# Optimization experiments

Hardware: AMD Instinct MI355X
Metric: run time of the kernel (lower is better)

Reference implementation:

```python
import jax, jax.numpy as jnp
import numpy as np

SHOT, WAY, DIM, Q, R = 5, 32, 640, 4096, 10
TEMP, L, DIV = 16.0, 2.0, 10.0
EPS = 1e-5


def _expmap0(x, c):
    # x: (..., d); c: broadcastable to (..., 1). Exponential map at origin + ball projection.
    sc = jnp.sqrt(c)
    n = jnp.maximum(jnp.linalg.norm(x, axis=-1, keepdims=True), EPS)
    y = jnp.tanh(sc * n) * x / (sc * n)
    ny = jnp.maximum(jnp.linalg.norm(y, axis=-1, keepdims=True), EPS)
    maxn = (1.0 - 1e-3) / sc
    return jnp.where(ny > maxn, y * (maxn / ny), y)


def _dist(x, y, c):
    # Poincare distance: 2/sqrt(c) * artanh(sqrt(c) * ||mobius_add(-x, y)||)
    u = -x
    uy = jnp.sum(u * y, -1, keepdims=True)
    u2 = jnp.sum(u * u, -1, keepdims=True)
    y2 = jnp.sum(y * y, -1, keepdims=True)
    num = (1.0 + 2.0 * c * uy + c * y2) * u + (1.0 - c * u2) * y
    den = jnp.maximum(1.0 + 2.0 * c * uy + c * c * u2 * y2, EPS)
    n = jnp.linalg.norm(num / den, axis=-1, keepdims=True)
    sc = jnp.sqrt(c)
    arg = jnp.clip(sc * n, 0.0, 1.0 - EPS)
    return ((2.0 / sc) * jnp.arctanh(arg))[..., 0]


def setup_inputs() -> dict:
    key = jax.random.key(0)
    ks = jax.random.split(key, 8)
    f = lambda k, s: jax.random.normal(k, s, dtype=jnp.float32)
    z = lambda s: jnp.zeros(s, jnp.float32)
    return {
        "data_shot": f(ks[0], (SHOT * WAY, DIM)),
        "data_query": f(ks[1], (Q, DIM)),
        "W1": f(ks[2], (2 * DIM, 128)) * 0.05, "b1": z((128,)),
        "W2": f(ks[3], (128, 64)) * 0.05, "b2": z((64,)),
        "W3": f(ks[4], (64, 5)) * 0.05, "b3": z((5,)),
        "Wr1": f(ks[5], (2 * R + 2, R)) * 0.05, "br1": z((R,)),
        "Wr2": f(ks[6], (R, R + 1)) * 0.05, "br2": z((R + 1,)),
    }


def reference(data_shot, data_query, W1, b1, W2, b2, W3, b3, Wr1, br1, Wr2, br2):
    # --- episode stats + per-class curvature controller ---
    all_data = jnp.concatenate([data_shot, data_query], 0).mean(0)      # (dim,)
    protos = data_shot.reshape(SHOT, WAY, DIM).mean(0)                  # (way, dim)
    ctrl_in = jnp.concatenate([protos, jnp.broadcast_to(all_data, (WAY, DIM))], 1)
    h = jax.nn.relu(ctrl_in @ W1 + b1)
    h = jax.nn.relu(h @ W2 + b2)
    cand = jnp.arange(1, 6, dtype=jnp.float32) * (L / DIV)              # 5 curvature candidates
    c = jax.nn.softmax(h @ W3 + b3, axis=-1) @ cand                     # (way,) positive curvature

    # --- hyperbolic projection + per-class proto-query distances (vectorized over classes) ---
    proto_p = _expmap0(protos, c[:, None])                              # (way, dim)
    query_p = _expmap0(data_query[None], c[:, None, None])              # (way, Q, dim)
    dis_mat = _dist(proto_p[:, None, :], query_p, c[:, None, None])     # (way, Q)

    # --- sort + gather-based rerank features ---
    idx = jnp.argsort(dis_mat, axis=1)
    idx_near, idx_far = idx[:, :R], idx[:, R:]
    n_i_d = jnp.take_along_axis(dis_mat, idx_near, 1)                   # (way, R)
    o_i_d = jnp.take_along_axis(dis_mat, idx_far, 1).mean(1)            # (way,)
    dT = dis_mat.T                                                      # (Q, way)
    Gnear = dT[idx_near]                                                # (way, R, way): [i,k,j] = dis_mat[j, idx_near[i,k]]
    n_o_d = (Gnear.sum(-1) - n_i_d) / (WAY - 1)                         # (way, R)
    Gfar = dT[idx_far]                                                  # (way, Q-R, way)
    ii = jnp.arange(WAY)
    mlt = (ii[None, :] < ii[:, None]).astype(dis_mat.dtype)             # j < i
    mgt = (ii[None, :] > ii[:, None]).astype(dis_mat.dtype)             # j > i
    sumA = jnp.einsum('ikj,ij->i', Gfar, mlt)                           # gathered cols (rows before i)
    sumB = mgt @ dis_mat[:, R:].sum(1)                                  # raw cols R: (rows after i, as in source)
    o_o_d = (sumA + sumB) / ((WAY - 1) * (Q - R))

    # --- rerank controller MLP ---
    rr_in = jnp.concatenate([n_i_d, n_o_d, o_i_d[:, None], o_o_d[:, None]], 1)  # (way, 2R+2)
    hr = jax.nn.relu(rr_in @ Wr1 + br1)
    orr = hr @ Wr2 + br2                                                # (way, R+1)
    i_w = jax.nn.softmax(orr[:, :R], axis=-1)                           # (way, R)
    onw = jax.nn.sigmoid(orr[:, R])                                     # (way,)

    # --- proto update + final distances ---
    near_q = data_query[idx_near]                                       # (way, R, dim)
    wdq = (near_q * i_w[:, :, None]).sum(1)                             # (way, dim)
    tmp = protos * onw[:, None] + wdq * (1.0 - onw[:, None])
    test_proto = _expmap0(tmp, c[:, None])
    new_dis = _dist(test_proto[:, None, :], query_p, c[:, None, None])  # (way, Q)
    return -new_dis.T / TEMP                                            # (Q, way)
```

## Files before the change

kernel.cpp:

```cpp
#include <hip/hip_runtime.h>
#include <math.h>

#define NSHOT 5
#define WAY 32
#define DIM 640
#define NQ 4096
#define RNEAR 10

constexpr int OFF_PROTOS = 0;
constexpr int OFF_QPART  = 20480;
constexpr int OFF_C      = 102400;
constexpr int OFF_BETA   = 102432;
constexpr int OFF_S      = 102464;
constexpr int OFF_U      = 102496;
constexpr int OFF_NID    = 102528;
constexpr int OFF_RR     = 102848;
constexpr int OFF_SPC    = 103552;
constexpr int OFF_H1P    = 103584;
constexpr int OFF_TP     = 107680;
constexpr int OFF_G      = 128160;
constexpr int OFF_NIDX   = 259232;
constexpr int OFF_Q2D    = 259556;
constexpr int OFF_X2D    = 267748;
constexpr int OFF_X2D2   = 267812;
constexpr int OFF_P2RAW  = 267876;
constexpr int OFF_H1PART = 268000;

__device__ __forceinline__ double wave_sum_d(double v) {
#pragma unroll
  for (int o = 32; o > 0; o >>= 1) v += __shfl_down(v, o, 64);
  return v;
}

__device__ __forceinline__ double dist_hyp(double c, double xdotq, double u2, double q2) {
  const double EPSd = 1e-5;
  double sc = sqrt(c);
  double nq = sqrt(q2);
  double nf = fmax(nq, EPSd);
  double th = tanh(sc * nf);
  double al = th / (sc * nf);
  double ny = fmax(al * nq, EPSd);
  double mx = 0.999 / sc;
  if (ny > mx) al *= mx / ny;
  double y2 = al * al * q2;
  double uy = -al * xdotq;
  double A = 1.0 + 2.0 * c * uy + c * y2;
  double B = 1.0 - c * u2;
  double den = fmax(1.0 + 2.0 * c * uy + c * c * u2 * y2, EPSd);
  double num2 = fmax(A * A * u2 + 2.0 * A * B * uy + B * B * y2, 0.0);
  double n = sqrt(num2) / den;
  double arg = sc * n;
  const double CLIP = (double)(1.0f - 1e-5f);
  arg = fmin(fmax(arg, 0.0), CLIP);
  return (1.0 / sc) * log((1.0 + arg) / (1.0 - arg));
}

__device__ __forceinline__ float dist_f32(float c, float xdotq, float u2, float q2) {
  const float EPSf = 1e-5f;
  float sc = sqrtf(c);
  float nq = sqrtf(q2);
  float nf = fmaxf(nq, EPSf);
  float th = tanhf(sc * nf);
  float al = th / (sc * nf);
  float ny = fmaxf(al * nq, EPSf);
  float mx = 0.999f / sc;
  if (ny > mx) al *= mx / ny;
  float y2 = al * al * q2;
  float uy = -al * xdotq;
  float A = 1.f + 2.f * c * uy + c * y2;
  float B = 1.f - c * u2;
  float den = fmaxf(1.f + 2.f * c * uy + c * c * u2 * y2, EPSf);
  float num2 = fmaxf(A * A * u2 + 2.f * A * B * uy + B * B * y2, 0.f);
  float n = sqrtf(num2) / den;
  float arg = sc * n;
  arg = fminf(fmaxf(arg, 0.f), 1.f - 1e-5f);
  return (1.f / sc) * logf((1.f + arg) / (1.f - arg));
}

__device__ __forceinline__ double expmap_scale(double c, double p2, double* u2out) {
  double sc = sqrt(c);
  double ntrue = sqrt(p2);
  double nf = fmax(ntrue, 1e-5);
  double th = tanh(sc * nf);
  double s0 = th / (sc * nf);
  double ny = fmax(s0 * ntrue, 1e-5);
  double mx = 0.999 / sc;
  if (ny > mx) s0 *= mx / ny;
  *u2out = s0 * s0 * p2;
  return s0;
}

__global__ __launch_bounds__(640) void k_fuse1(const float* __restrict__ Qm,
                                               const float* __restrict__ shot,
                                               const float* __restrict__ W1, float* ws) {
  __shared__ double q2w[32][10];
  __shared__ double psred[10];
  __shared__ float pr[DIM];
  __shared__ float h1pp[5][128];
  int b = blockIdx.x, t = threadIdx.x;
  int lane = t & 63, wid = t >> 6;
  float protoval = 0.f;
  if (b < WAY) {
    float s = 0.f;
#pragma unroll
    for (int s5 = 0; s5 < NSHOT; ++s5) s += shot[(size_t)(s5 * WAY + b) * DIM + t];
    protoval = s * 0.2f;
    pr[t] = protoval;
    ws[OFF_PROTOS + b * DIM + t] = protoval;
    double pv2 = (double)protoval * protoval;
    pv2 = wave_sum_d(pv2);
    if (lane == 0) psred[wid] = pv2;
  }
  int r0 = b * 32;
  float colacc = 0.f;
  for (int r = 0; r < 32; ++r) {
    float v = Qm[(size_t)(r0 + r) * DIM + t];
    colacc += v;
    double sq = (double)v * v;
    sq = wave_sum_d(sq);
    if (lane == 0) q2w[r][wid] = sq;
  }
  ws[OFF_QPART + b * DIM + t] = colacc + 5.f * protoval;
  __syncthreads();
  if (t < 32) {
    double s = 0.0;
#pragma unroll
    for (int k = 0; k < 10; ++k) s += q2w[t][k];
    ((double*)(ws + OFF_Q2D))[r0 + t] = s;
  }
  if (b < WAY) {
    int n = t & 127, s = t >> 7;
    int k0 = s * 128;
    float acc = 0.f;
#pragma unroll 8
    for (int k = k0; k < k0 + 128; ++k) acc = fmaf(pr[k], W1[(size_t)k * 128 + n], acc);
    h1pp[s][n] = acc;
    __syncthreads();
    if (t < 128)
      ws[OFF_H1P + b * 128 + t] = h1pp[0][t] + h1pp[1][t] + h1pp[2][t] + h1pp[3][t] + h1pp[4][t];
    if (t == 0) {
      double p2 = 0.0;
#pragma unroll
      for (int k = 0; k < 10; ++k) p2 += psred[k];
      ((double*)(ws + OFF_P2RAW))[b] = p2;
    }
  }
}

__global__ __launch_bounds__(320) void k_amw1(const float* __restrict__ W1, float* ws) {
  __shared__ float part_am[4][80];
  __shared__ float am_s[80];
  __shared__ float h1part[2][128];
  int j = blockIdx.x, t = threadIdx.x;
  {
    int c = t % 80, pg = t / 80;
    const float* base = ws + OFF_QPART + j * 80 + c;
    int p0 = pg * 32;
    float a0 = 0.f, a1 = 0.f, a2 = 0.f, a3 = 0.f;
#pragma unroll 8
    for (int p = 0; p < 32; p += 4) {
      a0 += base[(size_t)(p0 + p + 0) * DIM];
      a1 += base[(size_t)(p0 + p + 1) * DIM];
      a2 += base[(size_t)(p0 + p + 2) * DIM];
      a3 += base[(size_t)(p0 + p + 3) * DIM];
    }
    part_am[pg][c] = (a0 + a1) + (a2 + a3);
  }
  __syncthreads();
  if (t < 80)
    am_s[t] = (part_am[0][t] + part_am[1][t] + part_am[2][t] + part_am[3][t]) * (1.f / 4256.f);
  __syncthreads();
  if (t < 256) {
    int n = t & 127, kh = t >> 7;
    int kbase = j * 80 + kh * 40;
    float acc = 0.f;
#pragma unroll 8
    for (int k = 0; k < 40; ++k)
      acc = fmaf(am_s[kh * 40 + k], W1[(size_t)(DIM + kbase + k) * 128 + n], acc);
    h1part[kh][n] = acc;
  }
  __syncthreads();
  if (t < 128) ws[OFF_H1PART + j * 128 + t] = h1part[0][t] + h1part[1][t];
}

__global__ __launch_bounds__(128) void k_ctrl2(const float* __restrict__ b1,
                                               const float* __restrict__ W2, const float* __restrict__ b2,
                                               const float* __restrict__ W3, const float* __restrict__ b3,
                                               float* ws) {
  __shared__ float h1s[128];
  __shared__ float h2p[2][64];
  __shared__ float h2s[64], lg[5];
  int w = blockIdx.x, t = threadIdx.x;
  {
    float a = ws[OFF_H1P + w * 128 + t] + b1[t];
#pragma unroll
    for (int j = 0; j < 8; ++j) a += ws[OFF_H1PART + j * 128 + t];
    h1s[t] = fmaxf(a, 0.f);
  }
  __syncthreads();
  {
    int n = t & 63, kh = t >> 6;
    int k0 = kh * 64;
    float acc = 0.f;
#pragma unroll 8
    for (int k = 0; k < 64; ++k)
      acc = fmaf(h1s[k0 + k], W2[(size_t)(k0 + k) * 64 + n], acc);
    h2p[kh][n] = acc;
  }
  __syncthreads();
  if (t < 64) h2s[t] = fmaxf(h2p[0][t] + h2p[1][t] + b2[t], 0.f);
  __syncthreads();
  if (t < 5) {
    float acc = b3[t];
    for (int k = 0; k < 64; ++k) acc = fmaf(h2s[k], W3[k * 5 + t], acc);
    lg[t] = acc;
  }
  __syncthreads();
  if (t == 0) {
    double m = lg[0];
    for (int i = 1; i < 5; ++i) m = fmax(m, (double)lg[i]);
    double se = 0.0, cv = 0.0;
    for (int i = 0; i < 5; ++i) { double e = exp((double)lg[i] - m); se += e; cv += e * 0.2 * (double)(i + 1); }
    double c = cv / se;
    ws[OFF_C + w] = (float)c;
    double p2 = ((const double*)(ws + OFF_P2RAW))[w];
    double u2;
    double beta = expmap_scale(c, p2, &u2);
    ws[OFF_BETA + w] = (float)beta;
    ((double*)(ws + OFF_X2D))[w] = u2;
  }
}

#define GEMM_COMPUTE2(BUF)                                            \
  {                                                                   \
    const float* qr = &S[BUF][q][0];                                  \
    const float* x0r = &S[BUF][16 + w0][0];                           \
    const float* x1r = &S[BUF][16 + w1][0];                           \
    _Pragma("unroll")                                                 \
    for (int kk = 0; kk < 64; kk += 4) {                              \
      float4 qv = *(const float4*)(qr + kk);                          \
      float4 x0v = *(const float4*)(x0r + kk);                        \
      float4 x1v = *(const float4*)(x1r + kk);                       \
      c0x = fmaf(qv.x, x0v.x, c0x); c0y = fmaf(qv.y, x0v.y, c0y);     \
      c0z = fmaf(qv.z, x0v.z, c0z); c0w = fmaf(qv.w, x0v.w, c0w);     \
      c1x = fmaf(qv.x, x1v.x, c1x); c1y = fmaf(qv.y, x1v.y, c1y);     \
      c1z = fmaf(qv.z, x1v.z, c1z); c1w = fmaf(qv.w, x1v.w, c1w);     \
    }                                                                 \
  }

__global__ __launch_bounds__(256) void k_gemm(const float* __restrict__ X, const float* __restrict__ Qm,
                                              float* __restrict__ ws, int mode, float* __restrict__ out) {
  __shared__ float S[2][48][68];
  int t = threadIdx.x;
  int q0 = blockIdx.x * 16;
  int rr = t >> 4, qd = t & 15;
  const float* srcA = Qm + (size_t)(q0 + rr) * DIM + qd * 4;
  const float* srcB = X + (size_t)rr * DIM + qd * 4;
  const float* srcC = X + (size_t)(rr + 16) * DIM + qd * 4;
  float4 a0 = *(const float4*)srcA;
  float4 a1 = *(const float4*)srcB;
  float4 a2 = *(const float4*)srcC;
  *(float4*)&S[0][rr][qd * 4] = a0;
  *(float4*)&S[0][16 + rr][qd * 4] = a1;
  *(float4*)&S[0][32 + rr][qd * 4] = a2;
  __syncthreads();
  a0 = *(const float4*)(srcA + 64);
  a1 = *(const float4*)(srcB + 64);
  a2 = *(const float4*)(srcC + 64);
  float4 b0 = {0.f,0.f,0.f,0.f}, b1 = b0, b2 = b0;
  int q = t & 15, wp = t >> 4;
  int w0 = wp * 2, w1 = wp * 2 + 1;
  float c0x = 0.f, c0y = 0.f, c0z = 0.f, c0w = 0.f;
  float c1x = 0.f, c1y = 0.f, c1z = 0.f, c1w = 0.f;
#pragma unroll
  for (int c = 0; c < 10; c += 2) {
    GEMM_COMPUTE2(0)
    if (c + 2 < 10) {
      size_t kc = (size_t)(c + 2) * 64;
      b0 = *(const float4*)(srcA + kc);
      b1 = *(const float4*)(srcB + kc);
      b2 = *(const float4*)(srcC + kc);
    }
    if (c + 1 < 10) {
      *(float4*)&S[1][rr][qd * 4] = a0;
      *(float4*)&S[1][16 + rr][qd * 4] = a1;
      *(float4*)&S[1][32 + rr][qd * 4] = a2;
      __syncthreads();
      GEMM_COMPUTE2(1)
      if (c + 3 < 10) {
        size_t kc = (size_t)(c + 3) * 64;
        a0 = *(const float4*)(srcA + kc);
        a1 = *(const float4*)(srcB + kc);
        a2 = *(const float4*)(srcC + kc);
      }
      if (c + 2 < 10) {
        *(float4*)&S[0][rr][qd * 4] = b0;
        *(float4*)&S[0][16 + rr][qd * 4] = b1;
        *(float4*)&S[0][32 + rr][qd * 4] = b2;
        __syncthreads();
      }
    }
  }
  float acc0 = (c0x + c0y) + (c0z + c0w);
  float acc1 = (c1x + c1y) + (c1z + c1w);
  int qq = q0 + q;
  const double* q2d = (const double*)(ws + OFF_Q2D);
  if (mode == 0) {
    const double* x2d = (const double*)(ws + OFF_X2D);
    float q2f = (float)q2d[qq];
    float d0 = dist_f32(ws[OFF_C + w0], ws[OFF_BETA + w0] * acc0, (float)x2d[w0], q2f);
    float d1 = dist_f32(ws[OFF_C + w1], ws[OFF_BETA + w1] * acc1, (float)x2d[w1], q2f);
    ws[OFF_G + (size_t)w0 * NQ + qq] = d0;
    ws[OFF_G + (size_t)w1 * NQ + qq] = d1;
  } else {
    const double* u2arr = (const double*)(ws + OFF_X2D2);
    double q2 = q2d[qq];
    double d0 = dist_hyp((double)ws[OFF_C + w0], (double)acc0, u2arr[w0], q2);
    double d1 = dist_hyp((double)ws[OFF_C + w1], (double)acc1, u2arr[w1], q2);
    out[(size_t)qq * WAY + w0] = (float)(-d0 / 16.0);
    out[(size_t)qq * WAY + w1] = (float)(-d1 / 16.0);
  }
}

__global__ __launch_bounds__(1024) void k_topkA(float* __restrict__ ws) {
  __shared__ double sredS[16], sredU[16];
  __shared__ float cval[160];
  __shared__ int cidx[160];
  __shared__ float qvsh[RNEAR];
  __shared__ int qjsh[RNEAR];
  __shared__ float colsh[RNEAR][33];
  __shared__ float pcpart[RNEAR];
  int w = blockIdx.x, t = threadIdx.x;
  int lane = t & 63, wid = t >> 6;
  int* nidx = (int*)(ws + OFF_NIDX);
  const float* gb = ws + OFF_G + (size_t)w * NQ;
  float v0 = gb[t], v1 = gb[1024 + t], v2 = gb[2048 + t], v3 = gb[3072 + t];
  unsigned tk = 0;
  double s = (double)v0 + (double)v1 + (double)v2 + (double)v3;
  double u = (t < RNEAR) ? (double)v0 : 0.0;
  s = wave_sum_d(s);
  u = wave_sum_d(u);
  if (lane == 0) { sredS[wid] = s; sredU[wid] = u; }
  for (int r = 0; r < RNEAR; ++r) {
    float lv = INFINITY; int li = 0x7fffffff;
    if (!(tk & 1u) && (v0 < lv || (v0 == lv && t < li)))        { lv = v0; li = t; }
    if (!(tk & 2u) && (v1 < lv || (v1 == lv && 1024 + t < li))) { lv = v1; li = 1024 + t; }
    if (!(tk & 4u) && (v2 < lv || (v2 == lv && 2048 + t < li))) { lv = v2; li = 2048 + t; }
    if (!(tk & 8u) && (v3 < lv || (v3 == lv && 3072 + t < li))) { lv = v3; li = 3072 + t; }
#pragma unroll
    for (int o = 32; o > 0; o >>= 1) {
      float ov = __shfl_xor(lv, o, 64);
      int oi = __shfl_xor(li, o, 64);
      if (ov < lv || (ov == lv && oi < li)) { lv = ov; li = oi; }
    }
    if (lane == 0) { cval[wid * RNEAR + r] = lv; cidx[wid * RNEAR + r] = li; }
    if ((li & 1023) == t) tk |= 1u << (li >> 10);
  }
  __syncthreads();
  if (t == 0) {
    double S = 0.0, U = 0.0;
    for (int k = 0; k < 16; ++k) { S += sredS[k]; U += sredU[k]; }
    ws[OFF_S + w] = (float)S;
    ws[OFF_U + w] = (float)U;
  }
  if (t < 64) {
    float c0 = cval[t], c1 = cval[t + 64];
    int i0 = cidx[t], i1 = cidx[t + 64];
    float c2 = (t < 32) ? cval[t + 128] : INFINITY;
    int i2 = (t < 32) ? cidx[t + 128] : 0x7fffffff;
    unsigned m = 0;
    for (int r = 0; r < RNEAR; ++r) {
      float lv = INFINITY; int li = 0x7fffffff;
      if (!(m & 1u) && (c0 < lv || (c0 == lv && i0 < li))) { lv = c0; li = i0; }
      if (!(m & 2u) && (c1 < lv || (c1 == lv && i1 < li))) { lv = c1; li = i1; }
      if (!(m & 4u) && (c2 < lv || (c2 == lv && i2 < li))) { lv = c2; li = i2; }
#pragma unroll
      for (int o = 32; o > 0; o >>= 1) {
        float ov = __shfl_xor(lv, o, 64);
        int oi = __shfl_xor(li, o, 64);
        if (ov < lv || (ov == lv && oi < li)) { lv = ov; li = oi; }
      }
      if (lane == 0) { qvsh[r] = lv; qjsh[r] = li; }
      if (i0 == li) m |= 1u;
      if (i1 == li) m |= 2u;
      if (i2 == li) m |= 4u;
    }
  }
  __syncthreads();
  if (t < WAY * RNEAR) {
    int j = t >> 5, w2 = t & 31;
    colsh[j][w2] = ws[OFF_G + (size_t)w2 * NQ + qjsh[j]];
  }
  __syncthreads();
  if (t < RNEAR) {
    double cs = 0.0, pc = 0.0;
    for (int w2 = 0; w2 < WAY; ++w2) {
      float dv = colsh[t][w2];
      cs += dv;
      if (w2 < w) pc += dv;
    }
    ws[OFF_RR + w * 22 + t] = qvsh[t];
    ws[OFF_RR + w * 22 + RNEAR + t] = (float)((cs - qvsh[t]) / (double)(WAY - 1));
    ws[OFF_NID + w * RNEAR + t] = qvsh[t];
    nidx[w * RNEAR + t] = qjsh[t];
    pcpart[t] = (float)pc;
  }
  __syncthreads();
  if (t == 0) {
    double spc = 0.0, sn = 0.0;
    for (int j = 0; j < RNEAR; ++j) { spc += pcpart[j]; sn += qvsh[j]; }
    double S = (double)ws[OFF_S + w];
    ws[OFF_RR + w * 22 + 20] = (float)((S - sn) / (double)(NQ - RNEAR));
    ws[OFF_SPC + w] = (float)spc;
  }
}

__global__ __launch_bounds__(640) void k_refB(const float* __restrict__ Qm,
                                              const float* __restrict__ Wr1, const float* __restrict__ br1,
                                              const float* __restrict__ Wr2, const float* __restrict__ br2,
                                              float* __restrict__ ws) {
  __shared__ float Ssh[WAY], Ush[WAY];
  __shared__ float rrl[22];
  __shared__ int qj[RNEAR];
  __shared__ float hr[RNEAR], orsh[11], iw[RNEAR];
  __shared__ float onw_sh;
  __shared__ double p2red[10];
  __shared__ double gshd;
  int w = blockIdx.x, t = threadIdx.x;
  int lane = t & 63, wid = t >> 6;
  const int* nidx = (const int*)(ws + OFF_NIDX);
  if (t < WAY) { Ssh[t] = ws[OFF_S + t]; Ush[t] = ws[OFF_U + t]; }
  if (t >= 64 && t < 64 + 22) rrl[t - 64] = ws[OFF_RR + w * 22 + (t - 64)];
  if (t >= 96 && t < 96 + RNEAR) qj[t - 96] = nidx[w * RNEAR + (t - 96)];
  __syncthreads();
  if (t == 0) {
    double pref = 0.0, suf = 0.0;
    for (int j = 0; j < w; ++j) pref += (double)Ssh[j];
    for (int j = w + 1; j < WAY; ++j) suf += (double)Ssh[j] - (double)Ush[j];
    double spc = (double)ws[OFF_SPC + w];
    rrl[21] = (float)((pref - spc + suf) / ((double)(WAY - 1) * (double)(NQ - RNEAR)));
  }
  __syncthreads();
  if (t < RNEAR) {
    float a = br1[t];
    for (int k = 0; k < 22; ++k) a = fmaf(rrl[k], Wr1[k * RNEAR + t], a);
    hr[t] = fmaxf(a, 0.f);
  }
  __syncthreads();
  if (t < 11) {
    float a = br2[t];
    for (int k = 0; k < RNEAR; ++k) a = fmaf(hr[k], Wr2[k * 11 + t], a);
    orsh[t] = a;
  }
  __syncthreads();
  if (t == 0) {
    double m = orsh[0];
    for (int i = 1; i < RNEAR; ++i) m = fmax(m, (double)orsh[i]);
    double se = 0.0; double e[RNEAR];
    for (int i = 0; i < RNEAR; ++i) { e[i] = exp((double)orsh[i] - m); se += e[i]; }
    for (int i = 0; i < RNEAR; ++i) iw[i] = (float)(e[i] / se);
    onw_sh = (float)(1.0 / (1.0 + exp(-(double)orsh[10])));
  }
  __syncthreads();
  float onwv = onw_sh;
  float wd = 0.f;
#pragma unroll
  for (int j = 0; j < RNEAR; ++j)
    wd = fmaf(Qm[(size_t)qj[j] * DIM + t], iw[j], wd);
  float a0 = ws[OFF_PROTOS + w * DIM + t] * onwv + wd * (1.f - onwv);
  double ls = (double)a0 * a0;
  ls = wave_sum_d(ls);
  if (lane == 0) p2red[wid] = ls;
  __syncthreads();
  if (t == 0) {
    double p2 = 0.0;
#pragma unroll
    for (int k = 0; k < 10; ++k) p2 += p2red[k];
    double u22;
    gshd = expmap_scale((double)ws[OFF_C + w], p2, &u22);
    ((double*)(ws + OFF_X2D2))[w] = u22;
  }
  __syncthreads();
  ws[OFF_TP + w * DIM + t] = (float)gshd * a0;
}

extern "C" void kernel_launch(void* const* d_in, const int* in_sizes, int n_in,
                              void* d_out, int out_size, void* d_ws, size_t ws_size,
                              hipStream_t stream) {
  (void)in_sizes; (void)n_in; (void)out_size; (void)ws_size;
  const float* shot = (const float*)d_in[0];
  const float* qry  = (const float*)d_in[1];
  const float* W1   = (const float*)d_in[2];
  const float* b1   = (const float*)d_in[3];
  const float* W2   = (const float*)d_in[4];
  const float* b2   = (const float*)d_in[5];
  const float* W3   = (const float*)d_in[6];
  const float* b3   = (const float*)d_in[7];
  const float* Wr1  = (const float*)d_in[8];
  const float* br1  = (const float*)d_in[9];
  const float* Wr2  = (const float*)d_in[10];
  const float* br2  = (const float*)d_in[11];
  float* ws = (float*)d_ws;
  float* out = (float*)d_out;

  hipLaunchKernelGGL(k_fuse1, dim3(128), dim3(640), 0, stream, qry, shot, W1, ws);
  hipLaunchKernelGGL(k_amw1,  dim3(8), dim3(320), 0, stream, W1, ws);
  hipLaunchKernelGGL(k_ctrl2, dim3(32), dim3(128), 0, stream, b1, W2, b2, W3, b3, ws);
  hipLaunchKernelGGL(k_gemm,  dim3(256), dim3(256), 0, stream, ws + OFF_PROTOS, qry, ws, 0, out);
  hipLaunchKernelGGL(k_topkA, dim3(32), dim3(1024), 0, stream, ws);
  hipLaunchKernelGGL(k_refB,  dim3(32), dim3(640), 0, stream, qry, Wr1, br1, Wr2, br2, ws);
  hipLaunchKernelGGL(k_gemm,  dim3(256), dim3(256), 0, stream, ws + OFF_TP, qry, ws, 1, out);
}
```

Before: 80.92 us.

## Fuse controller MLP into last-arriving k_amw1 block; use fp32 final distance

Merges the k_ctrl2 kernel into k_amw1 through an atomic arrival counter. The last of the 8 blocks does the layer-2/3 MLP and softmax curvature for all 32 classes, which removes one kernel launch. The final-distance path in the second gemm switches from double-precision dist_hyp to the fp32 dist_f32, cutting costly fp64 transcendentals. The trade-offs are serial tail work in a single block and possible precision loss in the output distances.

```diff
diff --git a/kernel.cpp b/kernel.cpp
--- a/kernel.cpp
+++ b/kernel.cpp
@@ -25,6 +25,7 @@
 constexpr int OFF_X2D2   = 267812;
 constexpr int OFF_P2RAW  = 267876;
 constexpr int OFF_H1PART = 268000;
+constexpr int OFF_CNT    = 269024;
 
 __device__ __forceinline__ double wave_sum_d(double v) {
 #pragma unroll
@@ -32,27 +33,11 @@
   return v;
 }
 
-__device__ __forceinline__ double dist_hyp(double c, double xdotq, double u2, double q2) {
-  const double EPSd = 1e-5;
-  double sc = sqrt(c);
-  double nq = sqrt(q2);
-  double nf = fmax(nq, EPSd);
-  double th = tanh(sc * nf);
-  double al = th / (sc * nf);
-  double ny = fmax(al * nq, EPSd);
-  double mx = 0.999 / sc;
-  if (ny > mx) al *= mx / ny;
-  double y2 = al * al * q2;
-  double uy = -al * xdotq;
-  double A = 1.0 + 2.0 * c * uy + c * y2;
-  double B = 1.0 - c * u2;
-  double den = fmax(1.0 + 2.0 * c * uy + c * c * u2 * y2, EPSd);
-  double num2 = fmax(A * A * u2 + 2.0 * A * B * uy + B * B * y2, 0.0);
-  double n = sqrt(num2) / den;
-  double arg = sc * n;
-  const double CLIP = (double)(1.0f - 1e-5f);
-  arg = fmin(fmax(arg, 0.0), CLIP);
-  return (1.0 / sc) * log((1.0 + arg) / (1.0 - arg));
+__device__ __forceinline__ float aloadf(const float* p) {
+  return __hip_atomic_load(p, __ATOMIC_RELAXED, __HIP_MEMORY_SCOPE_AGENT);
+}
+__device__ __forceinline__ int aloadi(const int* p) {
+  return __hip_atomic_load(p, __ATOMIC_RELAXED, __HIP_MEMORY_SCOPE_AGENT);
 }
 
 __device__ __forceinline__ float dist_f32(float c, float xdotq, float u2, float q2) {
@@ -145,14 +130,22 @@
       ((double*)(ws + OFF_P2RAW))[b] = p2;
     }
   }
-}
-
-__global__ __launch_bounds__(320) void k_amw1(const float* __restrict__ W1, float* ws) {
+  if (b == 0 && t == 0) ((int*)(ws + OFF_CNT))[0] = 0;
+}
+
+__global__ __launch_bounds__(640) void k_amw1(const float* __restrict__ W1, const float* __restrict__ b1,
+                                              const float* __restrict__ W2, const float* __restrict__ b2,
+                                              const float* __restrict__ W3, const float* __restrict__ b3,
+                                              float* ws) {
   __shared__ float part_am[4][80];
   __shared__ float am_s[80];
-  __shared__ float h1part[2][128];
+  __shared__ float h1part_l[2][128];
+  __shared__ int tailflag;
+  __shared__ float hp[8][128];
+  __shared__ float h1all[32][128];
+  __shared__ float h2all[32][64];
   int j = blockIdx.x, t = threadIdx.x;
-  {
+  if (t < 320) {
     int c = t % 80, pg = t / 80;
     const float* base = ws + OFF_QPART + j * 80 + c;
     int p0 = pg * 32;
@@ -177,46 +170,48 @@
 #pragma unroll 8
     for (int k = 0; k < 40; ++k)
       acc = fmaf(am_s[kh * 40 + k], W1[(size_t)(DIM + kbase + k) * 128 + n], acc);
-    h1part[kh][n] = acc;
-  }
-  __syncthreads();
-  if (t < 128) ws[OFF_H1PART + j * 128 + t] = h1part[0][t] + h1part[1][t];
-}
-
-__global__ __launch_bounds__(128) void k_ctrl2(const float* __restrict__ b1,
-                                               const float* __restrict__ W2, const float* __restrict__ b2,
-                                               const float* __restrict__ W3, const float* __restrict__ b3,
-                                               float* ws) {
-  __shared__ float h1s[128];
-  __shared__ float h2p[2][64];
-  __shared__ float h2s[64], lg[5];
-  int w = blockIdx.x, t = threadIdx.x;
-  {
-    float a = ws[OFF_H1P + w * 128 + t] + b1[t];
-#pragma unroll
-    for (int j = 0; j < 8; ++j) a += ws[OFF_H1PART + j * 128 + t];
-    h1s[t] = fmaxf(a, 0.f);
-  }
-  __syncthreads();
-  {
-    int n = t & 63, kh = t >> 6;
-    int k0 = kh * 64;
-    float acc = 0.f;
+    h1part_l[kh][n] = acc;
+  }
+  __syncthreads();
+  if (t < 128) ws[OFF_H1PART + j * 128 + t] = h1part_l[0][t] + h1part_l[1][t];
+  __threadfence();
+  __syncthreads();
+  if (t == 0) {
+    int old = atomicAdd((int*)(ws + OFF_CNT), 1);
+    tailflag = (old == 7);
+  }
+  __syncthreads();
+  if (!tailflag) return;
+  __threadfence();
+  for (int i = t; i < 8 * 128; i += 640)
+    hp[i >> 7][i & 127] = aloadf(ws + OFF_H1PART + i);
+  __syncthreads();
+  for (int i = t; i < WAY * 128; i += 640) {
+    int w = i >> 7, n = i & 127;
+    float a = ws[OFF_H1P + w * 128 + n] + b1[n];
+#pragma unroll
+    for (int k = 0; k < 8; ++k) a += hp[k][n];
+    h1all[w][n] = fmaxf(a, 0.f);
+  }
+  __syncthreads();
+  for (int i = t; i < WAY * 64; i += 640) {
+    int w = i >> 6, n = i & 63;
+    float acc = b2[n];
 #pragma unroll 8
-    for (int k = 0; k < 64; ++k)
-      acc = fmaf(h1s[k0 + k], W2[(size_t)(k0 + k) * 64 + n], acc);
-    h2p[kh][n] = acc;
-  }
-  __syncthreads();
-  if (t < 64) h2s[t] = fmaxf(h2p[0][t] + h2p[1][t] + b2[t], 0.f);
-  __syncthreads();
-  if (t < 5) {
-    float acc = b3[t];
-    for (int k = 0; k < 64; ++k) acc = fmaf(h2s[k], W3[k * 5 + t], acc);
-    lg[t] = acc;
-  }
-  __syncthreads();
-  if (t == 0) {
+    for (int k = 0; k < 128; ++k)
+      acc = fmaf(h1all[w][k], W2[(size_t)k * 64 + n], acc);
+    h2all[w][n] = fmaxf(acc, 0.f);
+  }
+  __syncthreads();
+  if (t < WAY) {
+    int w = t;
+    float lg[5];
+#pragma unroll
+    for (int r = 0; r < 5; ++r) {
+      float acc = b3[r];
+      for (int k = 0; k < 64; ++k) acc = fmaf(h2all[w][k], W3[k * 5 + r], acc);
+      lg[r] = acc;
+    }
     double m = lg[0];
     for (int i = 1; i < 5; ++i) m = fmax(m, (double)lg[i]);
     double se = 0.0, cv = 0.0;
@@ -267,7 +262,7 @@
   a0 = *(const float4*)(srcA + 64);
   a1 = *(const float4*)(srcB + 64);
   a2 = *(const float4*)(srcC + 64);
-  float4 b0 = {0.f,0.f,0.f,0.f}, b1 = b0, b2 = b0;
+  float4 b0 = {0.f,0.f,0.f,0.f}, b1v = b0, b2v = b0;
   int q = t & 15, wp = t >> 4;
   int w0 = wp * 2, w1 = wp * 2 + 1;
   float c0x = 0.f, c0y = 0.f, c0z = 0.f, c0w = 0.f;
@@ -278,8 +273,8 @@
     if (c + 2 < 10) {
       size_t kc = (size_t)(c + 2) * 64;
       b0 = *(const float4*)(srcA + kc);
-      b1 = *(const float4*)(srcB + kc);
-      b2 = *(const float4*)(srcC + kc);
+      b1v = *(const float4*)(srcB + kc);
+      b2v = *(const float4*)(srcC + kc);
     }
     if (c + 1 < 10) {
       *(float4*)&S[1][rr][qd * 4] = a0;
@@ -295,8 +290,8 @@
       }
       if (c + 2 < 10) {
         *(float4*)&S[0][rr][qd * 4] = b0;
-        *(float4*)&S[0][16 + rr][qd * 4] = b1;
-        *(float4*)&S[0][32 + rr][qd * 4] = b2;
+        *(float4*)&S[0][16 + rr][qd * 4] = b1v;
+        *(float4*)&S[0][32 + rr][qd * 4] = b2v;
         __syncthreads();
       }
     }
@@ -305,20 +300,19 @@
   float acc1 = (c1x + c1y) + (c1z + c1w);
   int qq = q0 + q;
   const double* q2d = (const double*)(ws + OFF_Q2D);
+  float q2f = (float)q2d[qq];
   if (mode == 0) {
     const double* x2d = (const double*)(ws + OFF_X2D);
-    float q2f = (float)q2d[qq];
     float d0 = dist_f32(ws[OFF_C + w0], ws[OFF_BETA + w0] * acc0, (float)x2d[w0], q2f);
     float d1 = dist_f32(ws[OFF_C + w1], ws[OFF_BETA + w1] * acc1, (float)x2d[w1], q2f);
     ws[OFF_G + (size_t)w0 * NQ + qq] = d0;
     ws[OFF_G + (size_t)w1 * NQ + qq] = d1;
   } else {
     const double* u2arr = (const double*)(ws + OFF_X2D2);
-    double q2 = q2d[qq];
-    double d0 = dist_hyp((double)ws[OFF_C + w0], (double)acc0, u2arr[w0], q2);
-    double d1 = dist_hyp((double)ws[OFF_C + w1], (double)acc1, u2arr[w1], q2);
-    out[(size_t)qq * WAY + w0] = (float)(-d0 / 16.0);
-    out[(size_t)qq * WAY + w1] = (float)(-d1 / 16.0);
+    float d0 = dist_f32(ws[OFF_C + w0], acc0, (float)u2arr[w0], q2f);
+    float d1 = dist_f32(ws[OFF_C + w1], acc1, (float)u2arr[w1], q2f);
+    out[(size_t)qq * WAY + w0] = -d0 * (1.f / 16.f);
+    out[(size_t)qq * WAY + w1] = -d1 * (1.f / 16.f);
   }
 }
 
@@ -504,8 +498,7 @@
   float* out = (float*)d_out;
 
   hipLaunchKernelGGL(k_fuse1, dim3(128), dim3(640), 0, stream, qry, shot, W1, ws);
-  hipLaunchKernelGGL(k_amw1,  dim3(8), dim3(320), 0, stream, W1, ws);
-  hipLaunchKernelGGL(k_ctrl2, dim3(32), dim3(128), 0, stream, b1, W2, b2, W3, b3, ws);
+  hipLaunchKernelGGL(k_amw1,  dim3(8), dim3(640), 0, stream, W1, b1, W2, b2, W3, b3, ws);
   hipLaunchKernelGGL(k_gemm,  dim3(256), dim3(256), 0, stream, ws + OFF_PROTOS, qry, ws, 0, out);
   hipLaunchKernelGGL(k_topkA, dim3(32), dim3(1024), 0, stream, ws);
   hipLaunchKernelGGL(k_refB,  dim3(32), dim3(640), 0, stream, qry, Wr1, br1, Wr2, br2, ws);
```

Result: slower. 92.53 us (+14.3%).
